# Performance work log

Hardware: AMD Instinct MI355X
Metric: run time of the kernel (lower is better)

The kernel has to match this reference:

```python
import jax, jax.numpy as jnp
import numpy as np

B = 65536
H = 128          # hidden_size
IN_BOT = 128     # input_bottom_size
IN_TOP = 128     # input_top_size
GATE_W = 4 * H + 1  # 513: 4 gate chunks + 1 boundary logit
HARD_A = 1.0
ROUND_TH = 0.5


def setup_inputs() -> dict:
    key = jax.random.key(0)
    ks = jax.random.split(key, 10)
    sd = 1.0 / np.sqrt(H)
    return {
        "h_bottom": jax.random.normal(ks[0], (B, IN_BOT), jnp.float32),
        "h":        jax.random.normal(ks[1], (B, H), jnp.float32),
        "h_top":    jax.random.normal(ks[2], (B, IN_TOP), jnp.float32),
        "c":        jax.random.normal(ks[3], (B, H), jnp.float32),
        "z":        jax.random.randint(ks[4], (B, 1), 0, 2).astype(jnp.float32),
        "z_bottom": jax.random.randint(ks[5], (B, 1), 0, 2).astype(jnp.float32),
        "W": jax.random.uniform(ks[6], (IN_BOT, GATE_W), jnp.float32, -sd, sd),
        "R": jax.random.uniform(ks[7], (H, GATE_W), jnp.float32, -sd, sd),
        "U": jax.random.uniform(ks[8], (IN_TOP, GATE_W), jnp.float32, -sd, sd),
        "b": jax.random.uniform(ks[9], (GATE_W,), jnp.float32, -sd, sd),
    }


def _hard_sigm(x, a=HARD_A):
    # HardSigm: clip((a*x + 1)/2, 0, 1)
    return jnp.clip((a * x + 1.0) * 0.5, 0.0, 1.0)


def _round_st(z_tilde, th=ROUND_TH):
    # threshold rounding with straight-through gradient (identity backward)
    hard = (z_tilde > th).astype(z_tilde.dtype)
    return z_tilde + jax.lax.stop_gradient(hard - z_tilde)


def reference(h_bottom, h, h_top, c, z, z_bottom, W, R, U, b):
    # fused gate pre-activations: [B, 4H+1]
    s = (h_bottom * z_bottom) @ W + h @ R + (h_top * z) @ U + b
    si = s[:, 0 * H:1 * H]
    sg = s[:, 1 * H:2 * H]
    so = s[:, 2 * H:3 * H]
    sf = s[:, 3 * H:4 * H]
    sz = s[:, 4 * H:4 * H + 1]
    i = jax.nn.sigmoid(si)
    g = jnp.tanh(sg)
    o = jax.nn.sigmoid(so)
    f = jax.nn.sigmoid(sf)
    ig = i * g
    # FLUSH if z==1; COPY if z==0 & z_bottom==0; UPDATE otherwise
    c_new = jnp.where(z == 1.0, ig, jnp.where(z_bottom == 0.0, c, c * f + ig))
    h_new = jnp.where((z == 0.0) & (z_bottom == 0.0), h, jnp.tanh(c_new) * o)
    z_new = _round_st(_hard_sigm(sz))
    return (h_new, c_new, z_new)
```

## Files before the change

kernel.cpp:

```cpp
#include <hip/hip_runtime.h>
#include <hip/hip_bf16.h>


#define MT   128
#define BK   32
#define NKC  12
#define NT   512
#define COFF 8388608
#define ZOFF 16777216

using short8 = __attribute__((ext_vector_type(8))) short;
using f32x4  = __attribute__((ext_vector_type(4))) float;

__device__ __forceinline__ unsigned short f2bf(float f) {
  union { float f; unsigned u; } v; v.f = f;
  unsigned r = (v.u + 0x7FFFu + ((v.u >> 16) & 1u)) >> 16;
  return (unsigned short)r;
}

__device__ __forceinline__ void async_copy16(const void* g, void* l) {
  __builtin_amdgcn_global_load_lds(
      (const __attribute__((address_space(1))) unsigned int*)g,
      (__attribute__((address_space(3))) unsigned int*)l, 16, 0, 0);
}

__device__ __forceinline__ float sigm(float x)     { return 1.f / (1.f + __expf(-x)); }
__device__ __forceinline__ float tanh_fast(float x){ return 1.f - 2.f / (1.f + __expf(2.f * x)); }

__global__ void prep_weights(const float* __restrict__ W, const float* __restrict__ R,
                             const float* __restrict__ U, unsigned short* __restrict__ Wt) {
  int idx = blockIdx.x * blockDim.x + threadIdx.x;
  if (idx >= NKC * 512 * 4) return;
  int up = idx & 3;
  int n  = (idx >> 2) & 511;
  int c  = idx >> 11;
  int ul = up ^ ((n >> 1) & 3);
  int k0 = c * 32 + ul * 8;
  const float* src; int kb;
  if (k0 < 128)      { src = W; kb = 0;   }
  else if (k0 < 256) { src = R; kb = 128; }
  else               { src = U; kb = 256; }
  const float* colp = src + (size_t)(k0 - kb) * 513 + n;
  unsigned short vs[8];
  #pragma unroll
  for (int j = 0; j < 8; ++j) vs[j] = f2bf(colp[j * 513]);
  uint4 o;
  o.x = (unsigned)vs[0] | ((unsigned)vs[1] << 16);
  o.y = (unsigned)vs[2] | ((unsigned)vs[3] << 16);
  o.z = (unsigned)vs[4] | ((unsigned)vs[5] << 16);
  o.w = (unsigned)vs[6] | ((unsigned)vs[7] << 16);
  reinterpret_cast<uint4*>(Wt)[idx] = o;
}

__global__ __launch_bounds__(512, 2)
void hmlstm_main(const float* __restrict__ hb, const float* __restrict__ hs,
                 const float* __restrict__ ht, const float* __restrict__ cs,
                 const float* __restrict__ zp, const float* __restrict__ zbp,
                 const float* __restrict__ W,  const float* __restrict__ R,
                 const float* __restrict__ U,  const float* __restrict__ b,
                 const unsigned short* __restrict__ Wt, float* __restrict__ out)
{
  __shared__ unsigned short ldsW[512 * BK];
  __shared__ unsigned short ldsA[2][MT * BK];
  __shared__ float  ldsWL[384];
  __shared__ double ldsSZ[NT];

  const int tid  = threadIdx.x;
  const int l    = tid & 63;
  const int wv   = tid >> 6;
  const int ws   = wv & 3;
  const int wr   = wv >> 2;
  const int q    = l >> 4;
  const int lr   = l & 15;
  const int row0 = blockIdx.x * MT;

  for (int k = tid; k < 384; k += NT) {
    ldsWL[k] = (k < 128) ? W[k * 513 + 512]
             : (k < 256) ? R[(k - 128) * 513 + 512]
                         : U[(k - 256) * 513 + 512];
  }

  const int m    = tid >> 2;
  const int p    = tid & 3;
  const int arow = row0 + m;
  const float zbv = zbp[arow];
  const float zv  = zp[arow];
  double szacc = 0.0;

  f32x4 acc[4][8];
  {
    f32x4 zf = {0.f, 0.f, 0.f, 0.f};
    #pragma unroll
    for (int i = 0; i < 4; ++i)
      #pragma unroll
      for (int j = 0; j < 8; ++j) acc[i][j] = zf;
  }

  const int aW = m * BK + ((p ^ ((m >> 1) & 3)) * 8);

  __syncthreads();

  auto stageA = [&](int kc, int buf) {
    const float* src  = (kc < 4) ? hb : (kc < 8) ? hs : ht;
    const float scale = (kc < 4) ? zbv : (kc < 8) ? 1.f : zv;
    const float* sp = src + (size_t)arow * 128 + (kc & 3) * 32 + p * 8;
    f32x4 v0 = *(const f32x4*)sp;
    f32x4 v1 = *(const f32x4*)(sp + 4);
    v0 *= scale; v1 *= scale;
    const float* wl = ldsWL + kc * 32 + p * 8;
    szacc += (double)v0.x * wl[0] + (double)v0.y * wl[1]
           + (double)v0.z * wl[2] + (double)v0.w * wl[3]
           + (double)v1.x * wl[4] + (double)v1.y * wl[5]
           + (double)v1.z * wl[6] + (double)v1.w * wl[7];
    uint4 pk;
    pk.x = (unsigned)f2bf(v0.x) | ((unsigned)f2bf(v0.y) << 16);
    pk.y = (unsigned)f2bf(v0.z) | ((unsigned)f2bf(v0.w) << 16);
    pk.z = (unsigned)f2bf(v1.x) | ((unsigned)f2bf(v1.y) << 16);
    pk.w = (unsigned)f2bf(v1.z) | ((unsigned)f2bf(v1.w) << 16);
    *(uint4*)&ldsA[buf][aW] = pk;
  };

  stageA(0, 0);

  for (int kc = 0; kc < NKC; ++kc) {
    const int cur = kc & 1, nxt = cur ^ 1;
    const unsigned short* gW = Wt + kc * (512 * BK);
    #pragma unroll
    for (int r = 0; r < 4; ++r) {
      int eo = (wv * 4 + r) * 512;
      async_copy16(gW + eo + l * 8, ldsW + eo);
    }
    if (kc < NKC - 1) stageA(kc + 1, nxt);
    __syncthreads();

    short8 bfr[8];
    #pragma unroll
    for (int tn = 0; tn < 8; ++tn) {
      int nc = (tn >> 1) * 128 + ws * 32 + (tn & 1) * 16 + lr;
      bfr[tn] = *(const short8*)&ldsW[nc * BK + ((q ^ ((nc >> 1) & 3)) * 8)];
    }
    #pragma unroll
    for (int s = 0; s < 4; ++s) {
      int mr = wr * 64 + s * 16 + lr;
      short8 af = *(const short8*)&ldsA[cur][mr * BK + ((q ^ ((mr >> 1) & 3)) * 8)];
      #pragma unroll
      for (int tn = 0; tn < 8; ++tn)
        acc[s][tn] = __builtin_amdgcn_mfma_f32_16x16x32_bf16(af, bfr[tn], acc[s][tn], 0, 0, 0);
    }
    __syncthreads();
  }

  ldsSZ[tid] = szacc;
  __syncthreads();
  if (tid < MT) {
    double ss = ldsSZ[tid * 4] + ldsSZ[tid * 4 + 1] + ldsSZ[tid * 4 + 2] + ldsSZ[tid * 4 + 3];
    float s = (float)ss + b[512];
    out[ZOFF + row0 + tid] = (s > 0.f) ? 1.f : 0.f;
  }

  float bias[2][4];
  #pragma unroll
  for (int th = 0; th < 2; ++th) {
    const int col = ws * 32 + th * 16 + lr;
    bias[th][0] = b[col];       bias[th][1] = b[128 + col];
    bias[th][2] = b[256 + col]; bias[th][3] = b[384 + col];
  }
  #pragma unroll
  for (int s = 0; s < 4; ++s) {
    #pragma unroll
    for (int r = 0; r < 4; ++r) {
      const int row = row0 + wr * 64 + s * 16 + q * 4 + r;
      const float zr  = zp[row];
      const float zbr = zbp[row];
      const size_t rowoff = (size_t)row * 128;
      #pragma unroll
      for (int th = 0; th < 2; ++th) {
        const int col = ws * 32 + th * 16 + lr;
        const size_t off = rowoff + col;
        float si = acc[s][0 + th][r] + bias[th][0];
        float sg = acc[s][2 + th][r] + bias[th][1];
        float so = acc[s][4 + th][r] + bias[th][2];
        float sf = acc[s][6 + th][r] + bias[th][3];
        float iv = sigm(si);
        float gv = tanh_fast(sg);
        float ov = sigm(so);
        float fv = sigm(sf);
        float ig = iv * gv;
        float cv = cs[off];
        float hv = hs[off];
        float cn = (zr == 1.f) ? ig : ((zbr == 0.f) ? cv : cv * fv + ig);
        float hn = (zr == 0.f && zbr == 0.f) ? hv : tanh_fast(cn) * ov;
        out[off]        = hn;
        out[COFF + off] = cn;
      }
    }
  }
}

extern "C" void kernel_launch(void* const* d_in, const int* in_sizes, int n_in,
                              void* d_out, int out_size, void* d_ws, size_t ws_size,
                              hipStream_t stream) {
  const float* hb  = (const float*)d_in[0];
  const float* hs  = (const float*)d_in[1];
  const float* ht  = (const float*)d_in[2];
  const float* cs  = (const float*)d_in[3];
  const float* zp  = (const float*)d_in[4];
  const float* zbp = (const float*)d_in[5];
  const float* W   = (const float*)d_in[6];
  const float* R   = (const float*)d_in[7];
  const float* U   = (const float*)d_in[8];
  const float* b   = (const float*)d_in[9];
  unsigned short* Wt = (unsigned short*)d_ws;
  float* out = (float*)d_out;

  prep_weights<<<dim3(96), dim3(256), 0, stream>>>(W, R, U, Wt);
  hmlstm_main<<<dim3(65536 / MT), dim3(NT), 0, stream>>>(
      hb, hs, ht, cs, zp, zbp, W, R, U, b, Wt, out);
}
```

Baseline: 252.8 us.

## Halve row tile, double-buffer weight chunks, and pipeline loads with one barrier

```diff
diff --git a/kernel.cpp b/kernel.cpp
--- a/kernel.cpp
+++ b/kernel.cpp
@@ -2,7 +2,7 @@
 #include <hip/hip_bf16.h>
 
 
-#define MT   128
+#define MT   64
 #define BK   32
 #define NKC  12
 #define NT   512
@@ -52,7 +52,7 @@
   reinterpret_cast<uint4*>(Wt)[idx] = o;
 }
 
-__global__ __launch_bounds__(512, 2)
+__global__ __launch_bounds__(NT, 4)
 void hmlstm_main(const float* __restrict__ hb, const float* __restrict__ hs,
                  const float* __restrict__ ht, const float* __restrict__ cs,
                  const float* __restrict__ zp, const float* __restrict__ zbp,
@@ -60,7 +60,7 @@
                  const float* __restrict__ U,  const float* __restrict__ b,
                  const unsigned short* __restrict__ Wt, float* __restrict__ out)
 {
-  __shared__ unsigned short ldsW[512 * BK];
+  __shared__ unsigned short ldsW[2][512 * BK];
   __shared__ unsigned short ldsA[2][MT * BK];
   __shared__ float  ldsWL[384];
   __shared__ double ldsSZ[NT];
@@ -80,80 +80,95 @@
                          : U[(k - 256) * 513 + 512];
   }
 
-  const int m    = tid >> 2;
-  const int p    = tid & 3;
+  const int m    = tid >> 3;
+  const int p    = tid & 7;
   const int arow = row0 + m;
   const float zbv = zbp[arow];
   const float zv  = zp[arow];
   double szacc = 0.0;
 
-  f32x4 acc[4][8];
+  f32x4 acc[2][8];
   {
     f32x4 zf = {0.f, 0.f, 0.f, 0.f};
     #pragma unroll
-    for (int i = 0; i < 4; ++i)
+    for (int i = 0; i < 2; ++i)
       #pragma unroll
       for (int j = 0; j < 8; ++j) acc[i][j] = zf;
   }
 
-  const int aW = m * BK + ((p ^ ((m >> 1) & 3)) * 8);
-
-  __syncthreads();
-
-  auto stageA = [&](int kc, int buf) {
-    const float* src  = (kc < 4) ? hb : (kc < 8) ? hs : ht;
-    const float scale = (kc < 4) ? zbv : (kc < 8) ? 1.f : zv;
-    const float* sp = src + (size_t)arow * 128 + (kc & 3) * 32 + p * 8;
-    f32x4 v0 = *(const f32x4*)sp;
-    f32x4 v1 = *(const f32x4*)(sp + 4);
-    v0 *= scale; v1 *= scale;
-    const float* wl = ldsWL + kc * 32 + p * 8;
-    szacc += (double)v0.x * wl[0] + (double)v0.y * wl[1]
-           + (double)v0.z * wl[2] + (double)v0.w * wl[3]
-           + (double)v1.x * wl[4] + (double)v1.y * wl[5]
-           + (double)v1.z * wl[6] + (double)v1.w * wl[7];
-    uint4 pk;
-    pk.x = (unsigned)f2bf(v0.x) | ((unsigned)f2bf(v0.y) << 16);
-    pk.y = (unsigned)f2bf(v0.z) | ((unsigned)f2bf(v0.w) << 16);
-    pk.z = (unsigned)f2bf(v1.x) | ((unsigned)f2bf(v1.y) << 16);
-    pk.w = (unsigned)f2bf(v1.z) | ((unsigned)f2bf(v1.w) << 16);
-    *(uint4*)&ldsA[buf][aW] = pk;
+  const int aW = m * BK + (((p >> 1) ^ ((m >> 1) & 3)) * 8) + (p & 1) * 4;
+  const size_t rowb = (size_t)arow * 128 + p * 4;
+
+  auto loadA = [&](int c) -> f32x4 {
+    const float* src = (c < 4) ? hb : (c < 8) ? hs : ht;
+    return *(const f32x4*)(src + rowb + (c & 3) * 32);
   };
-
-  stageA(0, 0);
-
-  for (int kc = 0; kc < NKC; ++kc) {
-    const int cur = kc & 1, nxt = cur ^ 1;
-    const unsigned short* gW = Wt + kc * (512 * BK);
+  auto consumeA = [&](int c, f32x4 v, int buf) {
+    const float scale = (c < 4) ? zbv : (c < 8) ? 1.f : zv;
+    v *= scale;
+    const float* wl = ldsWL + c * 32 + p * 4;
+    szacc += (double)v.x * wl[0] + (double)v.y * wl[1]
+           + (double)v.z * wl[2] + (double)v.w * wl[3];
+    uint2 pk;
+    pk.x = (unsigned)f2bf(v.x) | ((unsigned)f2bf(v.y) << 16);
+    pk.y = (unsigned)f2bf(v.z) | ((unsigned)f2bf(v.w) << 16);
+    *(uint2*)&ldsA[buf][aW] = pk;
+  };
+  auto stageW = [&](int c, int buf) {
+    const unsigned short* gW = Wt + c * (512 * BK);
     #pragma unroll
     for (int r = 0; r < 4; ++r) {
       int eo = (wv * 4 + r) * 512;
-      async_copy16(gW + eo + l * 8, ldsW + eo);
-    }
-    if (kc < NKC - 1) stageA(kc + 1, nxt);
-    __syncthreads();
-
-    short8 bfr[8];
+      async_copy16(gW + eo + l * 8, &ldsW[buf][eo]);
+    }
+  };
+
+  f32x4 a0 = loadA(0);
+  asm volatile("s_waitcnt lgkmcnt(0)" ::: "memory");
+  __builtin_amdgcn_s_barrier();
+  consumeA(0, a0, 0);
+  stageW(0, 0);
+  f32x4 ain = loadA(1);
+  stageW(1, 1);
+  asm volatile("s_waitcnt vmcnt(5)" ::: "memory");
+  asm volatile("s_waitcnt lgkmcnt(0)" ::: "memory");
+  __builtin_amdgcn_s_barrier();
+
+  #pragma unroll 1
+  for (int kc = 0; kc < NKC; ++kc) {
+    const int cur = kc & 1;
+    short8 af[2];
+    #pragma unroll
+    for (int s = 0; s < 2; ++s) {
+      int mr = wr * 32 + s * 16 + lr;
+      af[s] = *(const short8*)&ldsA[cur][mr * BK + ((q ^ ((mr >> 1) & 3)) * 8)];
+    }
     #pragma unroll
     for (int tn = 0; tn < 8; ++tn) {
       int nc = (tn >> 1) * 128 + ws * 32 + (tn & 1) * 16 + lr;
-      bfr[tn] = *(const short8*)&ldsW[nc * BK + ((q ^ ((nc >> 1) & 3)) * 8)];
-    }
-    #pragma unroll
-    for (int s = 0; s < 4; ++s) {
-      int mr = wr * 64 + s * 16 + lr;
-      short8 af = *(const short8*)&ldsA[cur][mr * BK + ((q ^ ((mr >> 1) & 3)) * 8)];
-      #pragma unroll
-      for (int tn = 0; tn < 8; ++tn)
-        acc[s][tn] = __builtin_amdgcn_mfma_f32_16x16x32_bf16(af, bfr[tn], acc[s][tn], 0, 0, 0);
-    }
-    __syncthreads();
+      short8 bf = *(const short8*)&ldsW[cur][nc * BK + ((q ^ ((nc >> 1) & 3)) * 8)];
+      acc[0][tn] = __builtin_amdgcn_mfma_f32_16x16x32_bf16(af[0], bf, acc[0][tn], 0, 0, 0);
+      acc[1][tn] = __builtin_amdgcn_mfma_f32_16x16x32_bf16(af[1], bf, acc[1][tn], 0, 0, 0);
+    }
+    if (kc < NKC - 1) {
+      consumeA(kc + 1, ain, cur ^ 1);
+      if (kc < NKC - 2) {
+        ain = loadA(kc + 2);
+        asm volatile("s_waitcnt vmcnt(1)" ::: "memory");
+      } else {
+        asm volatile("s_waitcnt vmcnt(0)" ::: "memory");
+      }
+      asm volatile("s_waitcnt lgkmcnt(0)" ::: "memory");
+      __builtin_amdgcn_s_barrier();
+      if (kc < NKC - 2) stageW(kc + 2, cur);
+    }
   }
 
   ldsSZ[tid] = szacc;
   __syncthreads();
   if (tid < MT) {
-    double ss = ldsSZ[tid * 4] + ldsSZ[tid * 4 + 1] + ldsSZ[tid * 4 + 2] + ldsSZ[tid * 4 + 3];
+    const double* pz = &ldsSZ[tid * 8];
+    double ss = ((pz[0] + pz[1]) + (pz[2] + pz[3])) + ((pz[4] + pz[5]) + (pz[6] + pz[7]));
     float s = (float)ss + b[512];
     out[ZOFF + row0 + tid] = (s > 0.f) ? 1.f : 0.f;
   }
@@ -166,10 +181,10 @@
     bias[th][2] = b[256 + col]; bias[th][3] = b[384 + col];
   }
   #pragma unroll
-  for (int s = 0; s < 4; ++s) {
+  for (int s = 0; s < 2; ++s) {
     #pragma unroll
     for (int r = 0; r < 4; ++r) {
-      const int row = row0 + wr * 64 + s * 16 + q * 4 + r;
+      const int row = row0 + wr * 32 + s * 16 + q * 4 + r;
       const float zr  = zp[row];
       const float zbr = zbp[row];
       const size_t rowoff = (size_t)row * 128;
```

Result: faster. 226.1 us (-10.6%).
